# Performance work log

Hardware: AMD Instinct MI355X
Metric: run time of the kernel (lower is better)

Reference implementation:

```python
import jax, jax.numpy as jnp
import numpy as np

N_NODES = 100000
N_EDGES = 1600000
IN_DIM = 48
HID = 128
BN_EPS = 1e-5


def _batchnorm(h, gamma, beta):
    # BatchNorm1d in training mode: batch mean, biased variance
    mu = jnp.mean(h, axis=0)
    var = jnp.mean(jnp.square(h - mu), axis=0)
    return (h - mu) * jax.lax.rsqrt(var + BN_EPS) * gamma + beta


def setup_inputs() -> dict:
    key = jax.random.key(0)
    ks = jax.random.split(key, 8)
    x = jax.random.normal(ks[0], (N_NODES, IN_DIM), dtype=jnp.float32)
    edge_index = jax.random.randint(ks[1], (2, N_EDGES), 0, N_NODES, dtype=jnp.int64)
    s1 = 1.0 / np.sqrt(IN_DIM)
    s2 = 1.0 / np.sqrt(HID)
    return {
        "x": x,
        "edge_index": edge_index,
        "W1": jax.random.uniform(ks[2], (HID, IN_DIM), jnp.float32, -s1, s1),
        "b1": jnp.zeros((HID,), jnp.float32),
        "g1": jnp.ones((HID,), jnp.float32),
        "be1": jnp.zeros((HID,), jnp.float32),
        "Wl": jax.random.uniform(ks[3], (HID, HID), jnp.float32, -s2, s2),
        "bl": jnp.zeros((HID,), jnp.float32),
        "Wr": jax.random.uniform(ks[4], (HID, HID), jnp.float32, -s2, s2),
        "g2": jnp.ones((HID,), jnp.float32),
        "be2": jnp.zeros((HID,), jnp.float32),
    }


def reference(x, edge_index, W1, b1, g1, be1, Wl, bl, Wr, g2, be2):
    # input projection: Linear -> BatchNorm -> ReLU
    h = x @ W1.T + b1                               # [N, HID]
    feat = jax.nn.relu(_batchnorm(h, g1, be1))      # [N, HID]

    # SAGEConv (mean aggregation): messages flow src -> dst
    src, dst = edge_index[0], edge_index[1]
    summed = jax.ops.segment_sum(feat[src], dst, num_segments=N_NODES)  # [N, HID]
    cnt = jax.ops.segment_sum(jnp.ones((N_EDGES,), jnp.float32), dst, num_segments=N_NODES)
    agg = summed / jnp.maximum(cnt, 1.0)[:, None]
    sage = agg @ Wl.T + bl + feat @ Wr.T            # lin_l(mean) + lin_r(self)

    out_feat = _batchnorm(sage, g2, be2)
    return (feat, out_feat)
```

## Files before the change

### kernel.cpp

```cpp
#include <hip/hip_runtime.h>
#include <hip/hip_bf16.h>

#define NN 100000
#define NE 1600000
#define INDIM 48
#define HID 128
#define K2 256
#define KP 64
#define BN_EPS 1e-5f

#define NBUK 782
#define BCAP 2816
#define CHUNK 8192
#define NBB 196
#define NPRJ 320

#define MT2 ((NN + 127) / 128)

#define BSTR 264
#define PSTR 72

typedef short s8v __attribute__((ext_vector_type(8)));
typedef float f4v __attribute__((ext_vector_type(4)));
typedef float f2v __attribute__((ext_vector_type(2)));

__device__ __forceinline__ unsigned short f2bf(float f) {
    __hip_bfloat16 b = __float2bfloat16(f);
    unsigned short u;
    __builtin_memcpy(&u, &b, 2);
    return u;
}
__device__ __forceinline__ float bflo(unsigned u) { return __uint_as_float(u << 16); }
__device__ __forceinline__ float bfhi(unsigned u) { return __uint_as_float(u & 0xffff0000u); }
__device__ __forceinline__ unsigned packbf(float lo, float hi) {
    return (unsigned)f2bf(lo) | ((unsigned)f2bf(hi) << 16);
}

__global__ __launch_bounds__(512) void k_prep_proj(const int* __restrict__ ei,
                                                   int* __restrict__ bcur,
                                                   unsigned int* __restrict__ bbuf,
                                                   const float* __restrict__ x,
                                                   const float* __restrict__ W1,
                                                   const float* __restrict__ b1,
                                                   unsigned short* __restrict__ Abuf,
                                                   float* __restrict__ colSum,
                                                   float* __restrict__ colSq) {
  union __align__(16) SMem {
    struct {
      int cnt[1024];
      int sc[2][1024];
      int ofs[1024];
      int gbase[1024];
      unsigned int stag[CHUNK];
      unsigned short sbkt[CHUNK];
    } p;
    struct {
      unsigned short Bsh[HID * PSTR];
      float redS[8][HID];
      float redQ[8][HID];
    } g;
  };
  __shared__ SMem sm;
  int tid = threadIdx.x;

  if (blockIdx.x < NBB) {
    int base = blockIdx.x * CHUNK;
    int lim = min(CHUNK, NE - base);
    sm.p.cnt[tid] = 0;
    sm.p.cnt[tid + 512] = 0;
    __syncthreads();
    unsigned rtag[CHUNK / 512];
    unsigned rbp[CHUNK / 512];
#pragma unroll
    for (int i = 0; i < CHUNK / 512; ++i) {
      int e = i * 512 + tid;
      rtag[i] = 0u;
      rbp[i] = 0xFFFFFFFFu;
      if (e < lim) {
        int s = ei[base + e];
        int d = ei[NE + base + e];
        s = min(max(s, 0), NN - 1);
        d = min(max(d, 0), NN - 1);
        int b = d >> 7;
        int pos = atomicAdd(&sm.p.cnt[b], 1);
        rtag[i] = (unsigned)s | ((unsigned)(d & 127) << 17);
        rbp[i] = ((unsigned)b << 16) | (unsigned)pos;
      }
    }
    __syncthreads();
    sm.p.sc[0][tid] = sm.p.cnt[tid];
    sm.p.sc[0][tid + 512] = sm.p.cnt[tid + 512];
    __syncthreads();
    int pp = 0;
    for (int d = 1; d < 1024; d <<= 1) {
      int a0 = sm.p.sc[pp][tid];
      int a1 = sm.p.sc[pp][tid + 512];
      if (tid >= d) a0 += sm.p.sc[pp][tid - d];
      a1 += sm.p.sc[pp][tid + 512 - d];
      sm.p.sc[pp ^ 1][tid] = a0;
      sm.p.sc[pp ^ 1][tid + 512] = a1;
      __syncthreads();
      pp ^= 1;
    }
    sm.p.ofs[tid] = sm.p.sc[pp][tid] - sm.p.cnt[tid];
    sm.p.ofs[tid + 512] = sm.p.sc[pp][tid + 512] - sm.p.cnt[tid + 512];
    if (tid < NBUK) sm.p.gbase[tid] = atomicAdd(&bcur[tid], sm.p.cnt[tid]);
    if (tid + 512 < NBUK) sm.p.gbase[tid + 512] = atomicAdd(&bcur[tid + 512], sm.p.cnt[tid + 512]);
    __syncthreads();
#pragma unroll
    for (int i = 0; i < CHUNK / 512; ++i) {
      unsigned bp = rbp[i];
      if (bp != 0xFFFFFFFFu) {
        int b = bp >> 16;
        int pos = bp & 0xFFFF;
        int slot = sm.p.ofs[b] + pos;
        sm.p.stag[slot] = rtag[i];
        sm.p.sbkt[slot] = (unsigned short)b;
      }
    }
    __syncthreads();
    for (int s = tid; s < lim; s += 512) {
      int b = sm.p.sbkt[s];
      int off = sm.p.gbase[b] + (s - sm.p.ofs[b]);
      if (off < BCAP) bbuf[(size_t)b * BCAP + off] = sm.p.stag[s];
    }
    return;
  }

  int bid2 = blockIdx.x - NBB;
  for (int i = tid; i < HID * KP; i += 512) {
    int j = i >> 6, k = i & (KP - 1);
    unsigned short val = (k < INDIM) ? f2bf(W1[j * INDIM + k]) : (unsigned short)0;
    unsigned boff = (unsigned)(k * 2) ^ ((((unsigned)j >> 3) & 7u) << 4);
    *(unsigned short*)((char*)&sm.g.Bsh[(size_t)j * PSTR] + boff) = val;
  }
  __syncthreads();
  int w = tid >> 6, l = tid & 63;
  int m16 = l & 15, q = l >> 4;
  unsigned sw = ((unsigned)m16 & 7u) << 4;
  float bcol[8];
#pragma unroll
  for (int nt = 0; nt < 8; ++nt) bcol[nt] = b1[m16 * 8 + nt];
  float ssum[8], ssq[8];
#pragma unroll
  for (int nt = 0; nt < 8; ++nt) { ssum[nt] = 0.f; ssq[nt] = 0.f; }
  f4v zero4 = {0.f, 0.f, 0.f, 0.f};
  s8v zero8 = {0, 0, 0, 0, 0, 0, 0, 0};
  for (int tile = bid2; tile < MT2; tile += NPRJ) {
    int row = tile * 128 + w * 16 + m16;
    bool rv = row < NN;
    const float* xr = x + (size_t)row * INDIM;
    f4v acc[8];
#pragma unroll
    for (int nt = 0; nt < 8; ++nt) acc[nt] = zero4;
#pragma unroll
    for (int kt = 0; kt < 2; ++kt) {
      int c0 = kt * 32 + q * 8;
      s8v a = zero8;
      if (rv && c0 < INDIM) {
        float4 v0 = *(const float4*)(xr + c0);
        float4 v1 = *(const float4*)(xr + c0 + 4);
        a[0] = (short)f2bf(v0.x); a[1] = (short)f2bf(v0.y);
        a[2] = (short)f2bf(v0.z); a[3] = (short)f2bf(v0.w);
        a[4] = (short)f2bf(v1.x); a[5] = (short)f2bf(v1.y);
        a[6] = (short)f2bf(v1.z); a[7] = (short)f2bf(v1.w);
      }
      unsigned base = (unsigned)(kt * 64 + q * 16) ^ sw;
#pragma unroll
      for (int nt = 0; nt < 8; ++nt) {
        int brow = m16 * 8 + nt;
        s8v b = *(const s8v*)((const char*)&sm.g.Bsh[(size_t)brow * PSTR] + base);
        acc[nt] = __builtin_amdgcn_mfma_f32_16x16x32_bf16(a, b, acc[nt], 0, 0, 0);
      }
    }
    int rbase = tile * 128 + w * 16 + q * 4;
#pragma unroll
    for (int r4 = 0; r4 < 4; ++r4) {
      int rr = rbase + r4;
      if (rr < NN) {
        float v0 = acc[0][r4] + bcol[0], v1 = acc[1][r4] + bcol[1];
        float v2 = acc[2][r4] + bcol[2], v3 = acc[3][r4] + bcol[3];
        float v4 = acc[4][r4] + bcol[4], v5 = acc[5][r4] + bcol[5];
        float v6 = acc[6][r4] + bcol[6], v7 = acc[7][r4] + bcol[7];
        uint4 o;
        o.x = packbf(v0, v1); o.y = packbf(v2, v3);
        o.z = packbf(v4, v5); o.w = packbf(v6, v7);
        *(uint4*)(Abuf + (size_t)rr * K2 + HID + m16 * 8) = o;
        ssum[0] += v0; ssq[0] = fmaf(v0, v0, ssq[0]);
        ssum[1] += v1; ssq[1] = fmaf(v1, v1, ssq[1]);
        ssum[2] += v2; ssq[2] = fmaf(v2, v2, ssq[2]);
        ssum[3] += v3; ssq[3] = fmaf(v3, v3, ssq[3]);
        ssum[4] += v4; ssq[4] = fmaf(v4, v4, ssq[4]);
        ssum[5] += v5; ssq[5] = fmaf(v5, v5, ssq[5]);
        ssum[6] += v6; ssq[6] = fmaf(v6, v6, ssq[6]);
        ssum[7] += v7; ssq[7] = fmaf(v7, v7, ssq[7]);
      }
    }
  }
#pragma unroll
  for (int nt = 0; nt < 8; ++nt) {
    float s = ssum[nt], qq = ssq[nt];
    s += __shfl_xor(s, 16);
    s += __shfl_xor(s, 32);
    qq += __shfl_xor(qq, 16);
    qq += __shfl_xor(qq, 32);
    if (q == 0) {
      sm.g.redS[w][m16 * 8 + nt] = s;
      sm.g.redQ[w][m16 * 8 + nt] = qq;
    }
  }
  __syncthreads();
  if (tid < HID) {
    float s = 0.f, qq = 0.f;
#pragma unroll
    for (int ww = 0; ww < 8; ++ww) { s += sm.g.redS[ww][tid]; qq += sm.g.redQ[ww][tid]; }
    atomicAdd(&colSum[tid], s);
    atomicAdd(&colSq[tid], qq);
  }
}

__global__ __launch_bounds__(256) void k_apply(float* __restrict__ feat,
                                               const float* __restrict__ colSum,
                                               const float* __restrict__ colSq,
                                               const float* __restrict__ g1,
                                               const float* __restrict__ be1,
                                               unsigned short* __restrict__ A,
                                               unsigned char* __restrict__ feat8) {
  __shared__ __align__(16) float sa[HID], sb[HID];
  int tid = threadIdx.x;
  if (tid < HID) {
    float mu = colSum[tid] * (1.0f / NN);
    float var = fmaxf(colSq[tid] * (1.0f / NN) - mu * mu, 0.f);
    float a = g1[tid] * rsqrtf(var + BN_EPS);
    sa[tid] = a;
    sb[tid] = be1[tid] - mu * a;
  }
  __syncthreads();
  int i = blockIdx.x * 256 + tid;
  if (i >= NN * 16) return;
  int r = i >> 4, c8 = (i & 15) << 3;
  unsigned short* ap = A + (size_t)r * K2 + HID + c8;
  uint4 hv = *(const uint4*)ap;
  float4 a0 = *(const float4*)(sa + c8);
  float4 a1 = *(const float4*)(sa + c8 + 4);
  float4 b0 = *(const float4*)(sb + c8);
  float4 b1 = *(const float4*)(sb + c8 + 4);
  float f0 = fmaxf(fmaf(bflo(hv.x), a0.x, b0.x), 0.f);
  float f1 = fmaxf(fmaf(bfhi(hv.x), a0.y, b0.y), 0.f);
  float f2 = fmaxf(fmaf(bflo(hv.y), a0.z, b0.z), 0.f);
  float f3 = fmaxf(fmaf(bfhi(hv.y), a0.w, b0.w), 0.f);
  float f4 = fmaxf(fmaf(bflo(hv.z), a1.x, b1.x), 0.f);
  float f5 = fmaxf(fmaf(bfhi(hv.z), a1.y, b1.y), 0.f);
  float f6 = fmaxf(fmaf(bflo(hv.w), a1.z, b1.z), 0.f);
  float f7 = fmaxf(fmaf(bfhi(hv.w), a1.w, b1.w), 0.f);
  float4 o0 = {f0, f1, f2, f3}, o1 = {f4, f5, f6, f7};
  *(float4*)(feat + (size_t)r * HID + c8) = o0;
  *(float4*)(feat + (size_t)r * HID + c8 + 4) = o1;
  uint4 ob;
  ob.x = packbf(f0, f1);
  ob.y = packbf(f2, f3);
  ob.z = packbf(f4, f5);
  ob.w = packbf(f6, f7);
  *(uint4*)ap = ob;
  unsigned p0 = __builtin_amdgcn_cvt_pk_fp8_f32(f0, f1, 0u, false);
  p0 = __builtin_amdgcn_cvt_pk_fp8_f32(f2, f3, p0, true);
  unsigned p1 = __builtin_amdgcn_cvt_pk_fp8_f32(f4, f5, 0u, false);
  p1 = __builtin_amdgcn_cvt_pk_fp8_f32(f6, f7, p1, true);
  uint2 o8 = {p0, p1};
  *(uint2*)(feat8 + (size_t)r * HID + c8) = o8;
}

__global__ __launch_bounds__(512) void k_bucket_agg(const unsigned int* __restrict__ bbuf,
                                                    const int* __restrict__ bcnt,
                                                    const unsigned char* __restrict__ feat8,
                                                    unsigned short* __restrict__ Abuf) {
  __shared__ unsigned int lcsr[BCAP];
  __shared__ int cnt[128], ofs[128], cur[128];
  __shared__ int sc[2][128];
  int tid = threadIdx.x;
  int b = blockIdx.x;
  int m = min(bcnt[b], BCAP);
  int n0 = b << 7;
  int nb = min(128, NN - n0);
  if (tid < 128) cnt[tid] = 0;
  __syncthreads();
  const unsigned int* bp = bbuf + (size_t)b * BCAP;
  for (int s = tid; s < m; s += 512) {
    unsigned p = bp[s];
    atomicAdd(&cnt[(p >> 17) & 127], 1);
  }
  __syncthreads();
  if (tid < 128) sc[0][tid] = cnt[tid];
  __syncthreads();
  int pp = 0;
  for (int d = 1; d < 128; d <<= 1) {
    if (tid < 128) {
      int v = sc[pp][tid];
      if (tid >= d) v += sc[pp][tid - d];
      sc[pp ^ 1][tid] = v;
    }
    __syncthreads();
    pp ^= 1;
  }
  if (tid < 128) {
    int o = sc[pp][tid] - cnt[tid];
    ofs[tid] = o;
    cur[tid] = o;
  }
  __syncthreads();
  for (int s = tid; s < m; s += 512) {
    unsigned p = bp[s];
    int ld = (p >> 17) & 127;
    int pos = atomicAdd(&cur[ld], 1);
    lcsr[pos] = p & 0x1FFFF;
  }
  __syncthreads();
  int lane = tid & 31;
  int g = tid >> 5;
  int half = (lane >> 3) & 3;
  int l8 = lane & 7;
  for (int ln = g; ln < nb; ln += 16) {
    int deg = cnt[ln], beg = ofs[ln];
    float ac[16];
#pragma unroll
    for (int i = 0; i < 16; ++i) ac[i] = 0.f;
#pragma unroll 2
    for (int j = 0; j < deg; j += 4) {
      int idx = j + half;
      uint4 v = {0u, 0u, 0u, 0u};
      if (idx < deg) {
        int s = lcsr[beg + idx];
        v = *(const uint4*)(feat8 + (size_t)s * HID + l8 * 16);
      }
      f2v d;
      d = __builtin_amdgcn_cvt_pk_f32_fp8(v.x, false); ac[0] += d.x;  ac[1] += d.y;
      d = __builtin_amdgcn_cvt_pk_f32_fp8(v.x, true);  ac[2] += d.x;  ac[3] += d.y;
      d = __builtin_amdgcn_cvt_pk_f32_fp8(v.y, false); ac[4] += d.x;  ac[5] += d.y;
      d = __builtin_amdgcn_cvt_pk_f32_fp8(v.y, true);  ac[6] += d.x;  ac[7] += d.y;
      d = __builtin_amdgcn_cvt_pk_f32_fp8(v.z, false); ac[8] += d.x;  ac[9] += d.y;
      d = __builtin_amdgcn_cvt_pk_f32_fp8(v.z, true);  ac[10] += d.x; ac[11] += d.y;
      d = __builtin_amdgcn_cvt_pk_f32_fp8(v.w, false); ac[12] += d.x; ac[13] += d.y;
      d = __builtin_amdgcn_cvt_pk_f32_fp8(v.w, true);  ac[14] += d.x; ac[15] += d.y;
    }
#pragma unroll
    for (int i = 0; i < 16; ++i) {
      ac[i] += __shfl_xor(ac[i], 8);
      ac[i] += __shfl_xor(ac[i], 16);
    }
    if (half == 0) {
      float inv = 1.f / fmaxf((float)deg, 1.f);
      uint4 o0, o1;
      o0.x = packbf(ac[0] * inv, ac[1] * inv);
      o0.y = packbf(ac[2] * inv, ac[3] * inv);
      o0.z = packbf(ac[4] * inv, ac[5] * inv);
      o0.w = packbf(ac[6] * inv, ac[7] * inv);
      o1.x = packbf(ac[8] * inv, ac[9] * inv);
      o1.y = packbf(ac[10] * inv, ac[11] * inv);
      o1.z = packbf(ac[12] * inv, ac[13] * inv);
      o1.w = packbf(ac[14] * inv, ac[15] * inv);
      unsigned short* op = Abuf + (size_t)(n0 + ln) * K2 + l8 * 16;
      *(uint4*)op = o0;
      *(uint4*)(op + 8) = o1;
    }
  }
}

__global__ __launch_bounds__(512) void k_gemm(
    const unsigned short* __restrict__ A,
    const float* __restrict__ Wl, const float* __restrict__ Wr,
    const float* __restrict__ bl, unsigned short* __restrict__ sageb,
    float* __restrict__ colSum, float* __restrict__ colSq) {
  __shared__ __align__(16) unsigned short Bsh[HID * BSTR];
  __shared__ float redS[8][HID], redQ[8][HID];
  int tid = threadIdx.x;
  for (int i4 = tid; i4 < HID * K2 / 4; i4 += 512) {
    int i = i4 << 2;
    int j = i >> 8, k = i & (K2 - 1);
    const float* src = (k < HID) ? (Wl + j * HID + k) : (Wr + j * HID + (k - HID));
    float4 v = *(const float4*)src;
    uint2 u;
    u.x = packbf(v.x, v.y);
    u.y = packbf(v.z, v.w);
    unsigned boff = (unsigned)(k * 2) ^ ((((unsigned)j >> 3) & 7u) << 4);
    *(uint2*)((char*)&Bsh[(size_t)j * BSTR] + boff) = u;
  }
  __syncthreads();
  int w = tid >> 6, l = tid & 63;
  int m16 = l & 15, q = l >> 4;
  unsigned sw = ((unsigned)m16 & 7u) << 4;
  int tile = blockIdx.x;
  int row = tile * 128 + w * 16 + m16;
  bool rv = row < NN;
  f4v zero4 = {0.f, 0.f, 0.f, 0.f};
  s8v zero8 = {0, 0, 0, 0, 0, 0, 0, 0};
  float bcol[8];
#pragma unroll
  for (int nt = 0; nt < 8; ++nt) bcol[nt] = bl[m16 * 8 + nt];
  f4v acc[8];
#pragma unroll
  for (int nt = 0; nt < 8; ++nt) acc[nt] = zero4;
#pragma unroll
  for (int kt = 0; kt < 8; ++kt) {
    s8v a = zero8;
    if (rv) a = *(const s8v*)(A + (size_t)row * K2 + kt * 32 + q * 8);
    unsigned base = (unsigned)(kt * 64 + q * 16) ^ sw;
#pragma unroll
    for (int nt = 0; nt < 8; ++nt) {
      int brow = m16 * 8 + nt;
      s8v bfr = *(const s8v*)((const char*)&Bsh[(size_t)brow * BSTR] + base);
      acc[nt] = __builtin_amdgcn_mfma_f32_16x16x32_bf16(a, bfr, acc[nt], 0, 0, 0);
    }
  }
  int rbase = tile * 128 + w * 16 + q * 4;
  float ssum[8], ssq[8];
#pragma unroll
  for (int nt = 0; nt < 8; ++nt) { ssum[nt] = 0.f; ssq[nt] = 0.f; }
#pragma unroll
  for (int r4 = 0; r4 < 4; ++r4) {
    int rr = rbase + r4;
    if (rr < NN) {
      float v0 = acc[0][r4] + bcol[0], v1 = acc[1][r4] + bcol[1];
      float v2 = acc[2][r4] + bcol[2], v3 = acc[3][r4] + bcol[3];
      float v4 = acc[4][r4] + bcol[4], v5 = acc[5][r4] + bcol[5];
      float v6 = acc[6][r4] + bcol[6], v7 = acc[7][r4] + bcol[7];
      uint4 o;
      o.x = packbf(v0, v1); o.y = packbf(v2, v3);
      o.z = packbf(v4, v5); o.w = packbf(v6, v7);
      *(uint4*)(sageb + (size_t)rr * HID + m16 * 8) = o;
      ssum[0] += v0; ssq[0] = fmaf(v0, v0, ssq[0]);
      ssum[1] += v1; ssq[1] = fmaf(v1, v1, ssq[1]);
      ssum[2] += v2; ssq[2] = fmaf(v2, v2, ssq[2]);
      ssum[3] += v3; ssq[3] = fmaf(v3, v3, ssq[3]);
      ssum[4] += v4; ssq[4] = fmaf(v4, v4, ssq[4]);
      ssum[5] += v5; ssq[5] = fmaf(v5, v5, ssq[5]);
      ssum[6] += v6; ssq[6] = fmaf(v6, v6, ssq[6]);
      ssum[7] += v7; ssq[7] = fmaf(v7, v7, ssq[7]);
    }
  }
#pragma unroll
  for (int nt = 0; nt < 8; ++nt) {
    float s = ssum[nt], qq = ssq[nt];
    s += __shfl_xor(s, 16);
    s += __shfl_xor(s, 32);
    qq += __shfl_xor(qq, 16);
    qq += __shfl_xor(qq, 32);
    if (q == 0) {
      redS[w][m16 * 8 + nt] = s;
      redQ[w][m16 * 8 + nt] = qq;
    }
  }
  __syncthreads();
  if (tid < HID) {
    float s = 0.f, qq = 0.f;
#pragma unroll
    for (int ww = 0; ww < 8; ++ww) { s += redS[ww][tid]; qq += redQ[ww][tid]; }
    atomicAdd(&colSum[tid], s);
    atomicAdd(&colSq[tid], qq);
  }
}

__global__ __launch_bounds__(256) void k_bn_apply(const unsigned short* __restrict__ sageb,
                                                  float* __restrict__ out,
                                                  const float* __restrict__ colSum,
                                                  const float* __restrict__ colSq,
                                                  const float* __restrict__ g2,
                                                  const float* __restrict__ be2) {
  __shared__ __align__(16) float sa[HID], sb[HID];
  int tid = threadIdx.x;
  if (tid < HID) {
    float mu = colSum[tid] * (1.0f / NN);
    float var = fmaxf(colSq[tid] * (1.0f / NN) - mu * mu, 0.f);
    float a = g2[tid] * rsqrtf(var + BN_EPS);
    sa[tid] = a;
    sb[tid] = be2[tid] - mu * a;
  }
  __syncthreads();
  int i = blockIdx.x * 256 + tid;
  if (i >= NN * 16) return;
  int r = i >> 4, c8 = (i & 15) << 3;
  uint4 sv = *(const uint4*)(sageb + (size_t)r * HID + c8);
  float4 a0 = *(const float4*)(sa + c8);
  float4 a1 = *(const float4*)(sa + c8 + 4);
  float4 b0 = *(const float4*)(sb + c8);
  float4 b1 = *(const float4*)(sb + c8 + 4);
  float4 o0, o1;
  o0.x = fmaf(bflo(sv.x), a0.x, b0.x);
  o0.y = fmaf(bfhi(sv.x), a0.y, b0.y);
  o0.z = fmaf(bflo(sv.y), a0.z, b0.z);
  o0.w = fmaf(bfhi(sv.y), a0.w, b0.w);
  o1.x = fmaf(bflo(sv.z), a1.x, b1.x);
  o1.y = fmaf(bfhi(sv.z), a1.y, b1.y);
  o1.z = fmaf(bflo(sv.w), a1.z, b1.z);
  o1.w = fmaf(bfhi(sv.w), a1.w, b1.w);
  *(float4*)(out + (size_t)r * HID + c8) = o0;
  *(float4*)(out + (size_t)r * HID + c8 + 4) = o1;
}

extern "C" void kernel_launch(void* const* d_in, const int* in_sizes, int n_in,
                              void* d_out, int out_size, void* d_ws, size_t ws_size,
                              hipStream_t stream) {
  const float* x   = (const float*)d_in[0];
  const int*   ei  = (const int*)d_in[1];
  const float* W1  = (const float*)d_in[2];
  const float* b1  = (const float*)d_in[3];
  const float* g1  = (const float*)d_in[4];
  const float* be1 = (const float*)d_in[5];
  const float* Wl  = (const float*)d_in[6];
  const float* bl  = (const float*)d_in[7];
  const float* Wr  = (const float*)d_in[8];
  const float* g2  = (const float*)d_in[9];
  const float* be2 = (const float*)d_in[10];

  float* feat_out = (float*)d_out;
  float* out2     = (float*)d_out + (size_t)NN * HID;

  size_t off = 0;
  auto alloc = [&](size_t bytes) -> void* {
    void* p = (char*)d_ws + off;
    off += (bytes + 255) & ~(size_t)255;
    return p;
  };
  float*          stats = (float*)alloc(4 * HID * 4);
  int*            bcur  = (int*)alloc((size_t)NBUK * 4);
  unsigned short* Abuf  = (unsigned short*)alloc((size_t)NN * K2 * 2);
  unsigned char*  feat8 = (unsigned char*)alloc((size_t)NN * HID);
  unsigned short* sageb = (unsigned short*)alloc((size_t)NN * HID * 2);
  unsigned int*   bbuf  = (unsigned int*)alloc((size_t)NBUK * BCAP * 4);
  float* colSum1 = stats;
  float* colSq1  = stats + HID;
  float* colSum2 = stats + 2 * HID;
  float* colSq2  = stats + 3 * HID;

  hipMemsetAsync(stats, 0, 4 * HID * 4 + (size_t)NBUK * 4, stream);
  k_prep_proj<<<NBB + NPRJ, 512, 0, stream>>>(ei, bcur, bbuf, x, W1, b1, Abuf, colSum1, colSq1);
  k_apply<<<(NN * 16 + 255) / 256, 256, 0, stream>>>(feat_out, colSum1, colSq1, g1, be1, Abuf, feat8);
  k_bucket_agg<<<NBUK, 512, 0, stream>>>(bbuf, bcur, feat8, Abuf);
  k_gemm<<<MT2, 512, 0, stream>>>(Abuf, Wl, Wr, bl, sageb, colSum2, colSq2);
  k_bn_apply<<<(NN * 16 + 255) / 256, 256, 0, stream>>>(sageb, out2, colSum2, colSq2, g2, be2);
}
```

Measured before the change: 280.3 us.

## Compute first BatchNorm stats from input Gram matrix and fuse apply into projection

Adds a small kernel that computes the 48x48 Gram matrix and column sums of x with MFMA. The projection kernel then derives each hidden column's mean and variance analytically from W1, b1, Gx and sx. With the statistics known in advance, BN+ReLU and the fp32, bf16 and fp8 outputs are written straight from the projection epilogue, so the separate k_apply pass and its reread of the bf16 hidden buffer go away. The cost is an extra read of x, some per-block setup to compute Q, and possible precision loss from the E[h^2]-mu^2 form.

```diff
diff --git a/kernel.cpp b/kernel.cpp
--- a/kernel.cpp
+++ b/kernel.cpp
@@ -14,6 +14,7 @@
 #define CHUNK 8192
 #define NBB 196
 #define NPRJ 320
+#define GRAMB 391
 
 #define MT2 ((NN + 127) / 128)
 
@@ -34,6 +35,72 @@
 __device__ __forceinline__ float bfhi(unsigned u) { return __uint_as_float(u & 0xffff0000u); }
 __device__ __forceinline__ unsigned packbf(float lo, float hi) {
     return (unsigned)f2bf(lo) | ((unsigned)f2bf(hi) << 16);
+}
+__device__ __forceinline__ float rbf(float f) {
+    return __uint_as_float((unsigned)f2bf(f) << 16);
+}
+
+__global__ __launch_bounds__(256) void k_gram(const float* __restrict__ x,
+                                              float* __restrict__ Gx,
+                                              float* __restrict__ sx) {
+  __shared__ __align__(16) unsigned short slabT[48 * 136];
+  __shared__ float gred[48 * 48];
+  __shared__ float ssx[48];
+  int tid = threadIdx.x;
+  for (int e = tid; e < 48 * 48; e += 256) gred[e] = 0.f;
+  if (tid < 48) ssx[tid] = 0.f;
+  int l = tid & 63, w = tid >> 6;
+  int m16 = l & 15, q = l >> 4;
+  f4v acc[3][3];
+#pragma unroll
+  for (int a_ = 0; a_ < 3; ++a_)
+#pragma unroll
+    for (int b_ = 0; b_ < 3; ++b_) acc[a_][b_] = (f4v){0.f, 0.f, 0.f, 0.f};
+  for (int s = blockIdx.x; s < 2 * GRAMB; s += GRAMB) {
+    int R0 = s << 7;
+    __syncthreads();
+#pragma unroll
+    for (int it = 0; it < 6; ++it) {
+      int slot = it * 256 + tid;
+      int r = slot & 127;
+      int c4 = (slot >> 7) << 2;
+      float4 v = {0.f, 0.f, 0.f, 0.f};
+      int rr = R0 + r;
+      if (rr < NN) v = *(const float4*)(x + (size_t)rr * INDIM + c4);
+      slabT[(c4 + 0) * 136 + r] = f2bf(v.x);
+      slabT[(c4 + 1) * 136 + r] = f2bf(v.y);
+      slabT[(c4 + 2) * 136 + r] = f2bf(v.z);
+      slabT[(c4 + 3) * 136 + r] = f2bf(v.w);
+      atomicAdd(&ssx[c4 + 0], rbf(v.x));
+      atomicAdd(&ssx[c4 + 1], rbf(v.y));
+      atomicAdd(&ssx[c4 + 2], rbf(v.z));
+      atomicAdd(&ssx[c4 + 3], rbf(v.w));
+    }
+    __syncthreads();
+    s8v fr[3];
+#pragma unroll
+    for (int t = 0; t < 3; ++t)
+      fr[t] = *(const s8v*)(slabT + (16 * t + m16) * 136 + w * 32 + q * 8);
+#pragma unroll
+    for (int ti = 0; ti < 3; ++ti)
+#pragma unroll
+      for (int tj = 0; tj < 3; ++tj)
+        acc[ti][tj] = __builtin_amdgcn_mfma_f32_16x16x32_bf16(fr[ti], fr[tj], acc[ti][tj], 0, 0, 0);
+  }
+  __syncthreads();
+#pragma unroll
+  for (int ti = 0; ti < 3; ++ti)
+#pragma unroll
+    for (int tj = 0; tj < 3; ++tj)
+#pragma unroll
+      for (int r = 0; r < 4; ++r) {
+        int gi = 16 * ti + q * 4 + r;
+        int gj = 16 * tj + m16;
+        atomicAdd(&gred[gi * 48 + gj], acc[ti][tj][r]);
+      }
+  __syncthreads();
+  for (int e = tid; e < 48 * 48; e += 256) atomicAdd(&Gx[e], gred[e]);
+  if (tid < 48) atomicAdd(&sx[tid], ssx[tid]);
 }
 
 __global__ __launch_bounds__(512) void k_prep_proj(const int* __restrict__ ei,
@@ -42,9 +109,13 @@
                                                    const float* __restrict__ x,
                                                    const float* __restrict__ W1,
                                                    const float* __restrict__ b1,
+                                                   const float* __restrict__ g1,
+                                                   const float* __restrict__ be1,
+                                                   const float* __restrict__ Gx,
+                                                   const float* __restrict__ sxg,
+                                                   float* __restrict__ feat,
                                                    unsigned short* __restrict__ Abuf,
-                                                   float* __restrict__ colSum,
-                                                   float* __restrict__ colSq) {
+                                                   unsigned char* __restrict__ feat8) {
   union __align__(16) SMem {
     struct {
       int cnt[1024];
@@ -56,8 +127,11 @@
     } p;
     struct {
       unsigned short Bsh[HID * PSTR];
-      float redS[8][HID];
-      float redQ[8][HID];
+      float W1f[HID * 49];
+      float Glin[48 * 48];
+      float qpart[4][HID];
+      float sa[HID], sb[HID];
+      float sxl[48];
     } g;
   };
   __shared__ SMem sm;
@@ -134,16 +208,53 @@
     unsigned boff = (unsigned)(k * 2) ^ ((((unsigned)j >> 3) & 7u) << 4);
     *(unsigned short*)((char*)&sm.g.Bsh[(size_t)j * PSTR] + boff) = val;
   }
+  for (int i = tid; i < HID * INDIM; i += 512) {
+    int c = i / INDIM, k = i - c * INDIM;
+    sm.g.W1f[c * 49 + k] = rbf(W1[i]);
+  }
+  for (int i = tid; i < 48 * 48; i += 512) sm.g.Glin[i] = Gx[i];
+  if (tid < 48) sm.g.sxl[tid] = sxg[tid];
+  __syncthreads();
+  {
+    int c = tid & 127, part = tid >> 7;
+    const float* wrow = &sm.g.W1f[c * 49];
+    float accq = 0.f;
+    for (int i = 0; i < 48; ++i) {
+      float wi = wrow[i];
+      const float* gr = &sm.g.Glin[i * 48 + part * 12];
+#pragma unroll
+      for (int jj = 0; jj < 12; ++jj)
+        accq = fmaf(wi * wrow[part * 12 + jj], gr[jj], accq);
+    }
+    sm.g.qpart[part][c] = accq;
+  }
+  __syncthreads();
+  if (tid < HID) {
+    int c = tid;
+    const float* wrow = &sm.g.W1f[c * 49];
+    float Q = sm.g.qpart[0][c] + sm.g.qpart[1][c] + sm.g.qpart[2][c] + sm.g.qpart[3][c];
+    float wsx = 0.f;
+#pragma unroll
+    for (int k = 0; k < 48; ++k) wsx = fmaf(wrow[k], sm.g.sxl[k], wsx);
+    float b1c = b1[c];
+    float S1 = wsx + (float)NN * b1c;
+    float S2 = Q + 2.f * b1c * wsx + (float)NN * b1c * b1c;
+    float mu = S1 * (1.0f / NN);
+    float var = fmaxf(S2 * (1.0f / NN) - mu * mu, 0.f);
+    float a = g1[c] * rsqrtf(var + BN_EPS);
+    sm.g.sa[c] = a;
+    sm.g.sb[c] = (b1c - mu) * a + be1[c];
+  }
   __syncthreads();
   int w = tid >> 6, l = tid & 63;
   int m16 = l & 15, q = l >> 4;
   unsigned sw = ((unsigned)m16 & 7u) << 4;
-  float bcol[8];
-#pragma unroll
-  for (int nt = 0; nt < 8; ++nt) bcol[nt] = b1[m16 * 8 + nt];
-  float ssum[8], ssq[8];
-#pragma unroll
-  for (int nt = 0; nt < 8; ++nt) { ssum[nt] = 0.f; ssq[nt] = 0.f; }
+  float sac[8], sbc[8];
+#pragma unroll
+  for (int nt = 0; nt < 8; ++nt) {
+    sac[nt] = sm.g.sa[m16 * 8 + nt];
+    sbc[nt] = sm.g.sb[m16 * 8 + nt];
+  }
   f4v zero4 = {0.f, 0.f, 0.f, 0.f};
   s8v zero8 = {0, 0, 0, 0, 0, 0, 0, 0};
   for (int tile = bid2; tile < MT2; tile += NPRJ) {
@@ -178,96 +289,32 @@
     for (int r4 = 0; r4 < 4; ++r4) {
       int rr = rbase + r4;
       if (rr < NN) {
-        float v0 = acc[0][r4] + bcol[0], v1 = acc[1][r4] + bcol[1];
-        float v2 = acc[2][r4] + bcol[2], v3 = acc[3][r4] + bcol[3];
-        float v4 = acc[4][r4] + bcol[4], v5 = acc[5][r4] + bcol[5];
-        float v6 = acc[6][r4] + bcol[6], v7 = acc[7][r4] + bcol[7];
-        uint4 o;
-        o.x = packbf(v0, v1); o.y = packbf(v2, v3);
-        o.z = packbf(v4, v5); o.w = packbf(v6, v7);
-        *(uint4*)(Abuf + (size_t)rr * K2 + HID + m16 * 8) = o;
-        ssum[0] += v0; ssq[0] = fmaf(v0, v0, ssq[0]);
-        ssum[1] += v1; ssq[1] = fmaf(v1, v1, ssq[1]);
-        ssum[2] += v2; ssq[2] = fmaf(v2, v2, ssq[2]);
-        ssum[3] += v3; ssq[3] = fmaf(v3, v3, ssq[3]);
-        ssum[4] += v4; ssq[4] = fmaf(v4, v4, ssq[4]);
-        ssum[5] += v5; ssq[5] = fmaf(v5, v5, ssq[5]);
-        ssum[6] += v6; ssq[6] = fmaf(v6, v6, ssq[6]);
-        ssum[7] += v7; ssq[7] = fmaf(v7, v7, ssq[7]);
-      }
-    }
-  }
-#pragma unroll
-  for (int nt = 0; nt < 8; ++nt) {
-    float s = ssum[nt], qq = ssq[nt];
-    s += __shfl_xor(s, 16);
-    s += __shfl_xor(s, 32);
-    qq += __shfl_xor(qq, 16);
-    qq += __shfl_xor(qq, 32);
-    if (q == 0) {
-      sm.g.redS[w][m16 * 8 + nt] = s;
-      sm.g.redQ[w][m16 * 8 + nt] = qq;
-    }
-  }
-  __syncthreads();
-  if (tid < HID) {
-    float s = 0.f, qq = 0.f;
-#pragma unroll
-    for (int ww = 0; ww < 8; ++ww) { s += sm.g.redS[ww][tid]; qq += sm.g.redQ[ww][tid]; }
-    atomicAdd(&colSum[tid], s);
-    atomicAdd(&colSq[tid], qq);
-  }
-}
-
-__global__ __launch_bounds__(256) void k_apply(float* __restrict__ feat,
-                                               const float* __restrict__ colSum,
-                                               const float* __restrict__ colSq,
-                                               const float* __restrict__ g1,
-                                               const float* __restrict__ be1,
-                                               unsigned short* __restrict__ A,
-                                               unsigned char* __restrict__ feat8) {
-  __shared__ __align__(16) float sa[HID], sb[HID];
-  int tid = threadIdx.x;
-  if (tid < HID) {
-    float mu = colSum[tid] * (1.0f / NN);
-    float var = fmaxf(colSq[tid] * (1.0f / NN) - mu * mu, 0.f);
-    float a = g1[tid] * rsqrtf(var + BN_EPS);
-    sa[tid] = a;
-    sb[tid] = be1[tid] - mu * a;
-  }
-  __syncthreads();
-  int i = blockIdx.x * 256 + tid;
-  if (i >= NN * 16) return;
-  int r = i >> 4, c8 = (i & 15) << 3;
-  unsigned short* ap = A + (size_t)r * K2 + HID + c8;
-  uint4 hv = *(const uint4*)ap;
-  float4 a0 = *(const float4*)(sa + c8);
-  float4 a1 = *(const float4*)(sa + c8 + 4);
-  float4 b0 = *(const float4*)(sb + c8);
-  float4 b1 = *(const float4*)(sb + c8 + 4);
-  float f0 = fmaxf(fmaf(bflo(hv.x), a0.x, b0.x), 0.f);
-  float f1 = fmaxf(fmaf(bfhi(hv.x), a0.y, b0.y), 0.f);
-  float f2 = fmaxf(fmaf(bflo(hv.y), a0.z, b0.z), 0.f);
-  float f3 = fmaxf(fmaf(bfhi(hv.y), a0.w, b0.w), 0.f);
-  float f4 = fmaxf(fmaf(bflo(hv.z), a1.x, b1.x), 0.f);
-  float f5 = fmaxf(fmaf(bfhi(hv.z), a1.y, b1.y), 0.f);
-  float f6 = fmaxf(fmaf(bflo(hv.w), a1.z, b1.z), 0.f);
-  float f7 = fmaxf(fmaf(bfhi(hv.w), a1.w, b1.w), 0.f);
-  float4 o0 = {f0, f1, f2, f3}, o1 = {f4, f5, f6, f7};
-  *(float4*)(feat + (size_t)r * HID + c8) = o0;
-  *(float4*)(feat + (size_t)r * HID + c8 + 4) = o1;
-  uint4 ob;
-  ob.x = packbf(f0, f1);
-  ob.y = packbf(f2, f3);
-  ob.z = packbf(f4, f5);
-  ob.w = packbf(f6, f7);
-  *(uint4*)ap = ob;
-  unsigned p0 = __builtin_amdgcn_cvt_pk_fp8_f32(f0, f1, 0u, false);
-  p0 = __builtin_amdgcn_cvt_pk_fp8_f32(f2, f3, p0, true);
-  unsigned p1 = __builtin_amdgcn_cvt_pk_fp8_f32(f4, f5, 0u, false);
-  p1 = __builtin_amdgcn_cvt_pk_fp8_f32(f6, f7, p1, true);
-  uint2 o8 = {p0, p1};
-  *(uint2*)(feat8 + (size_t)r * HID + c8) = o8;
+        float f0 = fmaxf(fmaf(acc[0][r4], sac[0], sbc[0]), 0.f);
+        float f1 = fmaxf(fmaf(acc[1][r4], sac[1], sbc[1]), 0.f);
+        float f2 = fmaxf(fmaf(acc[2][r4], sac[2], sbc[2]), 0.f);
+        float f3 = fmaxf(fmaf(acc[3][r4], sac[3], sbc[3]), 0.f);
+        float f4 = fmaxf(fmaf(acc[4][r4], sac[4], sbc[4]), 0.f);
+        float f5 = fmaxf(fmaf(acc[5][r4], sac[5], sbc[5]), 0.f);
+        float f6 = fmaxf(fmaf(acc[6][r4], sac[6], sbc[6]), 0.f);
+        float f7 = fmaxf(fmaf(acc[7][r4], sac[7], sbc[7]), 0.f);
+        float4 o0 = {f0, f1, f2, f3}, o1 = {f4, f5, f6, f7};
+        *(float4*)(feat + (size_t)rr * HID + m16 * 8) = o0;
+        *(float4*)(feat + (size_t)rr * HID + m16 * 8 + 4) = o1;
+        uint4 ob;
+        ob.x = packbf(f0, f1);
+        ob.y = packbf(f2, f3);
+        ob.z = packbf(f4, f5);
+        ob.w = packbf(f6, f7);
+        *(uint4*)(Abuf + (size_t)rr * K2 + HID + m16 * 8) = ob;
+        unsigned p0 = __builtin_amdgcn_cvt_pk_fp8_f32(f0, f1, 0u, false);
+        p0 = __builtin_amdgcn_cvt_pk_fp8_f32(f2, f3, p0, true);
+        unsigned p1 = __builtin_amdgcn_cvt_pk_fp8_f32(f4, f5, 0u, false);
+        p1 = __builtin_amdgcn_cvt_pk_fp8_f32(f6, f7, p1, true);
+        uint2 o8 = {p0, p1};
+        *(uint2*)(feat8 + (size_t)rr * HID + m16 * 8) = o8;
+      }
+    }
+  }
 }
 
 __global__ __launch_bounds__(512) void k_bucket_agg(const unsigned int* __restrict__ bbuf,
@@ -520,20 +567,23 @@
     off += (bytes + 255) & ~(size_t)255;
     return p;
   };
-  float*          stats = (float*)alloc(4 * HID * 4);
+  const size_t statsFloats = 2 * HID + 48 * 48 + 48;
+  float*          stats = (float*)alloc(statsFloats * 4);
   int*            bcur  = (int*)alloc((size_t)NBUK * 4);
   unsigned short* Abuf  = (unsigned short*)alloc((size_t)NN * K2 * 2);
   unsigned char*  feat8 = (unsigned char*)alloc((size_t)NN * HID);
   unsigned short* sageb = (unsigned short*)alloc((size_t)NN * HID * 2);
   unsigned int*   bbuf  = (unsigned int*)alloc((size_t)NBUK * BCAP * 4);
-  float* colSum1 = stats;
-  float* colSq1  = stats + HID;
-  float* colSum2 = stats + 2 * HID;
-  float* colSq2  = stats + 3 * HID;
-
-  hipMemsetAsync(stats, 0, 4 * HID * 4 + (size_t)NBUK * 4, stream);
-  k_prep_proj<<<NBB + NPRJ, 512, 0, stream>>>(ei, bcur, bbuf, x, W1, b1, Abuf, colSum1, colSq1);
-  k_apply<<<(NN * 16 + 255) / 256, 256, 0, stream>>>(feat_out, colSum1, colSq1, g1, be1, Abuf, feat8);
+  float* colSum2 = stats;
+  float* colSq2  = stats + HID;
+  float* Gx      = stats + 2 * HID;
+  float* sx      = stats + 2 * HID + 48 * 48;
+  size_t statsPad = ((statsFloats * 4 + 255) & ~(size_t)255);
+
+  hipMemsetAsync(stats, 0, statsPad + (size_t)NBUK * 4, stream);
+  k_gram<<<GRAMB, 256, 0, stream>>>(x, Gx, sx);
+  k_prep_proj<<<NBB + NPRJ, 512, 0, stream>>>(ei, bcur, bbuf, x, W1, b1, g1, be1, Gx, sx,
+                                              feat_out, Abuf, feat8);
   k_bucket_agg<<<NBUK, 512, 0, stream>>>(bbuf, bcur, feat8, Abuf);
   k_gemm<<<MT2, 512, 0, stream>>>(Abuf, Wl, Wr, bl, sageb, colSum2, colSq2);
   k_bn_apply<<<(NN * 16 + 255) / 256, 256, 0, stream>>>(sageb, out2, colSum2, colSq2, g2, be2);
```

After: 345.7 us. 23.3% more time.
